# Performance work log

Hardware: AMD Instinct MI355X
Metric: run time of the kernel (lower is better)

The kernel has to match this reference:

```python
import jax, jax.numpy as jnp
import numpy as np

EMB_DIM = 1024
HEAD_SIZE = 128
B, T = 8, 2048


def setup_inputs() -> dict:
    key = jax.random.key(0)
    kx, kk, kq, kv = jax.random.split(key, 4)
    x = jax.random.normal(kx, (B, T, EMB_DIM), dtype=jnp.float32)
    # torch nn.Linear(emb_dim, head_size, bias=False): weight [head_size, emb_dim], y = x @ W.T
    # store transposed as [emb_dim, head_size] for direct matmul
    s = 1.0 / np.sqrt(EMB_DIM)
    Wk = jax.random.uniform(kk, (EMB_DIM, HEAD_SIZE), dtype=jnp.float32, minval=-s, maxval=s)
    Wq = jax.random.uniform(kq, (EMB_DIM, HEAD_SIZE), dtype=jnp.float32, minval=-s, maxval=s)
    Wv = jax.random.uniform(kv, (EMB_DIM, HEAD_SIZE), dtype=jnp.float32, minval=-s, maxval=s)
    return {"x": x, "Wk": Wk, "Wq": Wq, "Wv": Wv}


def reference(x, Wk, Wq, Wv):
    Bb, Tt, C = x.shape
    k = jnp.einsum('btc,ch->bth', x, Wk)
    q = jnp.einsum('btc,ch->bth', x, Wq)
    v = jnp.einsum('btc,ch->bth', x, Wv)
    # NOTE: original computes k @ q^T (not q @ k^T) and scales by C**-0.5 (C = emb_dim)
    wei = jnp.einsum('bih,bjh->bij', k, q) * (C ** -0.5)  # [B, T, T]
    causal = jnp.tril(jnp.ones((Tt, Tt), dtype=bool))
    wei = jnp.where(causal, wei, -jnp.inf)
    wei = jax.nn.softmax(wei, axis=-1)
    out = jnp.einsum('bij,bjh->bih', wei, v)  # [B, T, head_size]
    return out
```

## Files before the change

kernel.cpp:

```cpp
#include <hip/hip_runtime.h>
#include <hip/hip_bf16.h>
#include <stdint.h>

#define Bn 8
#define Tn 2048
#define Cn 1024
#define Hn 128

typedef __attribute__((ext_vector_type(8))) short short8;
typedef __attribute__((ext_vector_type(4))) short short4v;
typedef __attribute__((ext_vector_type(4))) float f32x4;
typedef __attribute__((ext_vector_type(4))) int int4v;

static __device__ __forceinline__ unsigned short f2bf(float f) {
    union { float f; unsigned int u; } v; v.f = f;
    return (unsigned short)((v.u + 0x7FFFu + ((v.u >> 16) & 1u)) >> 16);
}
static __device__ __forceinline__ float bf2f(unsigned short h) {
    union { unsigned int u; float f; } v; v.u = ((unsigned int)h) << 16;
    return v.f;
}

#define KSCALE 0.04508422f

#define BASE_BYTES (3u * Bn * Tn * Hn * 2u + 3u * Hn * Cn * 2u)
#define SLOT_SH 2080
#define NBLK_FA 576
#define UPB_FA 72
#define CCHUNK 8

__global__ __launch_bounds__(256) void wt_prep(const float* __restrict__ Wk,
                                               const float* __restrict__ Wq,
                                               const float* __restrict__ Wv,
                                               unsigned short* __restrict__ WT) {
    int z = blockIdx.y;
    const float* W = (z == 0) ? Wk : (z == 1) ? Wq : Wv;
    unsigned short* wt = WT + (size_t)z * Hn * Cn;
    int o = blockIdx.x * 256 + threadIdx.x;
    int d = o >> 10;
    int k = o & (Cn - 1);
    wt[o] = f2bf(W[k * Hn + d]);
}

__global__ __launch_bounds__(256) void proj4(const float* __restrict__ x,
                                             const unsigned short* __restrict__ WTb,
                                             unsigned short* __restrict__ Kb,
                                             unsigned short* __restrict__ Qb,
                                             unsigned short* __restrict__ VT) {
    __shared__ __align__(16) unsigned short Asm[2][32 * 32];
    __shared__ __align__(16) unsigned short Bsm[2][384 * 32];
    int tid = threadIdx.x;
    int lane = tid & 63, w = tid >> 6;
    int lr = lane & 15, lg = lane >> 4;
    int r0 = blockIdx.x * 32;

    f32x4 xreg;
    int4v breg[6];
    int xrow = tid >> 3, xk4 = (tid & 7) * 4;
    int brow = tid >> 2, bk8 = (tid & 3) * 8;
    auto LOADS = [&](int k0) {
        xreg = *(const f32x4*)(x + (size_t)(r0 + xrow) * Cn + k0 + xk4);
        #pragma unroll
        for (int i = 0; i < 6; ++i)
            breg[i] = *(const int4v*)(WTb + (size_t)(i * 64 + brow) * Cn + k0 + bk8);
    };
    auto WRITES = [&](int bb) {
        short4v av;
        av[0] = (short)f2bf(xreg[0]); av[1] = (short)f2bf(xreg[1]);
        av[2] = (short)f2bf(xreg[2]); av[3] = (short)f2bf(xreg[3]);
        *(short4v*)((char*)&Asm[bb][0] + xrow * 64 + xk4 * 2) = av;
        char* bbase = (char*)&Bsm[bb][0];
        #pragma unroll
        for (int i = 0; i < 6; ++i)
            *(int4v*)(bbase + (i * 64 + brow) * 64 + bk8 * 2) = breg[i];
    };

    f32x4 acc[2][6] = {};
    LOADS(0);
    WRITES(0);
    __syncthreads();
    int cur = 0;
    for (int ks = 0; ks < 32; ++ks) {
        if (ks < 31) LOADS((ks + 1) * 32);
        const char* ab = (const char*)&Asm[cur][0];
        const char* bbp = (const char*)&Bsm[cur][0];
        short8 af[2], bf[6];
        #pragma unroll
        for (int m = 0; m < 2; ++m)
            af[m] = *(const short8*)(ab + (m * 16 + lr) * 64 + lg * 16);
        #pragma unroll
        for (int c = 0; c < 6; ++c)
            bf[c] = *(const short8*)(bbp + (w * 96 + c * 16 + lr) * 64 + lg * 16);
        #pragma unroll
        for (int m = 0; m < 2; ++m)
            #pragma unroll
            for (int c = 0; c < 6; ++c)
                acc[m][c] = __builtin_amdgcn_mfma_f32_16x16x32_bf16(af[m], bf[c], acc[m][c], 0, 0, 0);
        if (ks < 31) WRITES(cur ^ 1);
        __syncthreads();
        cur ^= 1;
    }

    #pragma unroll
    for (int m = 0; m < 2; ++m)
        #pragma unroll
        for (int c = 0; c < 6; ++c) {
            int col = w * 96 + c * 16 + lr;
            int z = col >> 7, d = col & 127;
            if (z == 2) {
                int i = r0 + m * 16 + lg * 4;
                int bb = i >> 11, tt = i & 2047;
                short4v pv;
                pv[0] = (short)f2bf(acc[m][c][0]);
                pv[1] = (short)f2bf(acc[m][c][1]);
                pv[2] = (short)f2bf(acc[m][c][2]);
                pv[3] = (short)f2bf(acc[m][c][3]);
                *(short4v*)(VT + ((size_t)(bb * Hn + d) << 11) + tt) = pv;
            } else {
                unsigned short* outp = (z == 0) ? Kb : Qb;
                float sc = (z == 0) ? KSCALE : 1.0f;
                #pragma unroll
                for (int r = 0; r < 4; ++r) {
                    int i = r0 + m * 16 + lg * 4 + r;
                    outp[(size_t)i * Hn + d] = f2bf(acc[m][c][r] * sc);
                }
            }
        }
}

__global__ __launch_bounds__(512) void fattn8(const unsigned short* __restrict__ Kb,
                                              const unsigned short* __restrict__ Qb,
                                              const unsigned short* __restrict__ VT,
                                              unsigned short* __restrict__ accP) {
    __shared__ __align__(16) unsigned short Ksm[2][32 * 128];
    __shared__ __align__(16) unsigned short Vsm[2][128 * 32];
    __shared__ __align__(16) unsigned short pbuf[8][16][48];
    int tid = threadIdx.x, lane = tid & 63, w = tid >> 6;
    int lr = lane & 15, lg = lane >> 4;

    int cpx = gridDim.x >> 3;
    int u = ((int)blockIdx.x & 7) * cpx + ((int)blockIdx.x >> 3);
    int b = u / UPB_FA, rem = u - b * UPB_FA;
    int g = 0, p = 0;
    for (;;) {
        int P = (4 * g + 4 + CCHUNK - 1) / CCHUNK;
        if (rem < P) { p = rem; break; }
        rem -= P; ++g;
    }
    int nt = 4 * g + 4;
    int P = (nt + CCHUNK - 1) / CCHUNK;
    int q = nt / P, r = nt % P;
    int begin = p * q + (p < r ? p : r);
    int size = q + (p < r ? 1 : 0);

    int i0 = g * 128 + w * 16;
    int tmax = (i0 + 15) >> 5;
    const unsigned short* kb = Kb + (size_t)b * Tn * Hn;
    const unsigned short* qb = Qb + (size_t)b * Tn * Hn;
    const unsigned short* vt = VT + (size_t)b * Hn * Tn;

    short8 kf[4];
    #pragma unroll
    for (int kk = 0; kk < 4; ++kk)
        kf[kk] = *(const short8*)(kb + (size_t)(i0 + lr) * Hn + kk * 32 + lg * 8);

    int krow = tid >> 4, kcol = (tid & 15) * 8;
    int vrow = tid >> 2, vcol = (tid & 3) * 8;
    int4v kreg, vreg;
    auto LOADT = [&](int tt) {
        int j0 = tt * 32;
        kreg = *(const int4v*)(qb + (size_t)(j0 + krow) * Hn + kcol);
        vreg = *(const int4v*)(vt + (size_t)vrow * Tn + j0 + vcol);
    };
    auto WRITET = [&](int bb) {
        *(int4v*)((char*)&Ksm[bb][0] + krow * 256 + ((kcol * 2) ^ ((krow & 7) << 4))) = kreg;
        *(int4v*)((char*)&Vsm[bb][0] + vrow * 64 + vcol * 2) = vreg;
    };

    f32x4 acc[8] = {};
    float ssum[4] = {0.f, 0.f, 0.f, 0.f};

    LOADT(begin);
    WRITET(0);
    __syncthreads();
    int cur = 0;
    for (int ti = 0; ti < size; ++ti) {
        int tt = begin + ti;
        if (ti + 1 < size) LOADT(tt + 1);
        if (tt <= tmax) {
            int j0 = tt * 32;
            const char* kbp = (const char*)&Ksm[cur][0];
            const char* vbp = (const char*)&Vsm[cur][0];
            f32x4 sa0 = {}, sa1 = {};
            #pragma unroll
            for (int kk = 0; kk < 4; ++kk) {
                int row = lr;
                short8 qf = *(const short8*)(kbp + row * 256 + (((kk * 64) + lg * 16) ^ ((row & 7) << 4)));
                sa0 = __builtin_amdgcn_mfma_f32_16x16x32_bf16(kf[kk], qf, sa0, 0, 0, 0);
            }
            #pragma unroll
            for (int kk = 0; kk < 4; ++kk) {
                int row = 16 + lr;
                short8 qf = *(const short8*)(kbp + row * 256 + (((kk * 64) + lg * 16) ^ ((row & 7) << 4)));
                sa1 = __builtin_amdgcn_mfma_f32_16x16x32_bf16(kf[kk], qf, sa1, 0, 0, 0);
            }
            bool needmask = (j0 + 31 > i0);
            #pragma unroll
            for (int rr = 0; rr < 4; ++rr) {
                float v0 = sa0[rr], v1 = sa1[rr];
                if (needmask) {
                    int i = i0 + lg * 4 + rr;
                    if (j0 + lr > i)      v0 = -1e30f;
                    if (j0 + 16 + lr > i) v1 = -1e30f;
                }
                float p0 = __builtin_amdgcn_exp2f(v0);
                float p1 = __builtin_amdgcn_exp2f(v1);
                ssum[rr] += p0 + p1;
                pbuf[w][lg * 4 + rr][lr] = f2bf(p0);
                pbuf[w][lg * 4 + rr][16 + lr] = f2bf(p1);
            }
            short8 pf = *(const short8*)(&pbuf[w][lr][lg * 8]);
            #pragma unroll
            for (int n = 0; n < 8; ++n) {
                int row = n * 16 + lr;
                short8 vf = *(const short8*)(vbp + row * 64 + lg * 16);
                acc[n] = __builtin_amdgcn_mfma_f32_16x16x32_bf16(pf, vf, acc[n], 0, 0, 0);
            }
        }
        if (ti + 1 < size) WRITET(cur ^ 1);
        __syncthreads();
        cur ^= 1;
    }

    unsigned short* dst = accP + (size_t)u * 8 * SLOT_SH + (size_t)w * SLOT_SH;
    #pragma unroll
    for (int n = 0; n < 8; ++n) {
        short4v pv;
        pv[0] = (short)f2bf(acc[n][0]);
        pv[1] = (short)f2bf(acc[n][1]);
        pv[2] = (short)f2bf(acc[n][2]);
        pv[3] = (short)f2bf(acc[n][3]);
        *(short4v*)(dst + n * 256 + lane * 4) = pv;
    }
    #pragma unroll
    for (int rr = 0; rr < 4; ++rr) {
        float s = ssum[rr];
        s += __shfl_xor(s, 1);
        s += __shfl_xor(s, 2);
        s += __shfl_xor(s, 4);
        s += __shfl_xor(s, 8);
        if (lr == 0) ((float*)(dst + 2048))[lg * 4 + rr] = s;
    }
}

__global__ __launch_bounds__(256) void combine3(const unsigned short* __restrict__ accP,
                                                float* __restrict__ out) {
    int cpx = gridDim.x >> 3;
    int bidx = ((int)blockIdx.x & 7) * cpx + ((int)blockIdx.x >> 3);
    int b = bidx >> 7, tile = bidx & 127;
    int g = tile >> 3, wq = tile & 7;
    int ub = b * UPB_FA;
    for (int gg = 0; gg < g; ++gg) ub += (4 * gg + 4 + CCHUNK - 1) / CCHUNK;
    int nt = 4 * g + 4;
    int P = (nt + CCHUNK - 1) / CCHUNK;

    int tid = threadIdx.x;
    int row = tid >> 4;
    int c8 = (tid & 15) * 8;

    const unsigned short* base = accP + ((size_t)ub * 8 + wq) * SLOT_SH;
    const size_t pstr = (size_t)8 * SLOT_SH;
    float den = 0.f;
    for (int pp = 0; pp < P; ++pp) den += ((const float*)(base + pp * pstr + 2048))[row];
    float inv = 1.0f / den;

    int lgg = row >> 2, r4 = row & 3;
    float ov[8];
    #pragma unroll
    for (int cc = 0; cc < 8; ++cc) {
        int col = c8 + cc;
        int n = col >> 4, lrr = col & 15;
        int flat = n * 256 + (lgg * 16 + lrr) * 4 + r4;
        float s = 0.f;
        for (int pp = 0; pp < P; ++pp) s += bf2f(base[pp * pstr + flat]);
        ov[cc] = s * inv;
    }
    float* op = out + ((size_t)(b * Tn + tile * 16 + row)) * Hn + c8;
    *(f32x4*)op       = f32x4{ov[0], ov[1], ov[2], ov[3]};
    *(f32x4*)(op + 4) = f32x4{ov[4], ov[5], ov[6], ov[7]};
}

__global__ __launch_bounds__(256) void attn(const unsigned short* __restrict__ Kb,
                                            const unsigned short* __restrict__ Qb,
                                            const unsigned short* __restrict__ VT,
                                            float* __restrict__ out) {
    __shared__ unsigned short pbuf[4][16][32];
    __shared__ __align__(16) float accbuf[4][16][132];
    __shared__ float ssbuf[4][16];
    int lane = threadIdx.x & 63;
    int w = threadIdx.x >> 6;
    int b = blockIdx.y;
    int xb = blockIdx.x;
    int tile = (xb & 1) ? (127 - (xb >> 1)) : (xb >> 1);
    int i0 = tile * 16;
    int lr = lane & 15, lg = lane >> 4;

    const unsigned short* kb = Kb + (size_t)b * Tn * Hn;
    const unsigned short* qb = Qb + (size_t)b * Tn * Hn;
    const unsigned short* vt = VT + (size_t)b * Hn * Tn;

    short8 kf[4];
    #pragma unroll
    for (int kk = 0; kk < 4; ++kk)
        kf[kk] = *(const short8*)(kb + (size_t)(i0 + lr) * Hn + kk * 32 + lg * 8);

    f32x4 acc[8] = {};
    float ssum[4] = {0.f, 0.f, 0.f, 0.f};

    int nt = (i0 + 15) / 32 + 1;
    for (int tt = w; tt < nt; tt += 4) {
        int j0 = tt * 32;
        f32x4 sa0 = {}, sa1 = {};
        #pragma unroll
        for (int kk = 0; kk < 4; ++kk) {
            short8 q0 = *(const short8*)(qb + (size_t)(j0 + lr) * Hn + kk * 32 + lg * 8);
            sa0 = __builtin_amdgcn_mfma_f32_16x16x32_bf16(kf[kk], q0, sa0, 0, 0, 0);
        }
        #pragma unroll
        for (int kk = 0; kk < 4; ++kk) {
            short8 q1 = *(const short8*)(qb + (size_t)(j0 + 16 + lr) * Hn + kk * 32 + lg * 8);
            sa1 = __builtin_amdgcn_mfma_f32_16x16x32_bf16(kf[kk], q1, sa1, 0, 0, 0);
        }
        bool needmask = (j0 + 31 > i0);
        #pragma unroll
        for (int r = 0; r < 4; ++r) {
            float v0 = sa0[r], v1 = sa1[r];
            if (needmask) {
                int i = i0 + lg * 4 + r;
                if (j0 + lr > i)      v0 = -1e30f;
                if (j0 + 16 + lr > i) v1 = -1e30f;
            }
            float p0 = __builtin_amdgcn_exp2f(v0);
            float p1 = __builtin_amdgcn_exp2f(v1);
            ssum[r] += p0 + p1;
            pbuf[w][lg * 4 + r][lr] = f2bf(p0);
            pbuf[w][lg * 4 + r][16 + lr] = f2bf(p1);
        }
        short8 pf = *(const short8*)(&pbuf[w][lr][lg * 8]);
        #pragma unroll
        for (int n = 0; n < 8; ++n) {
            short8 vf = *(const short8*)(vt + (size_t)(n * 16 + lr) * Tn + j0 + lg * 8);
            acc[n] = __builtin_amdgcn_mfma_f32_16x16x32_bf16(pf, vf, acc[n], 0, 0, 0);
        }
    }

    #pragma unroll
    for (int r = 0; r < 4; ++r) {
        float s = ssum[r];
        s += __shfl_xor(s, 1);
        s += __shfl_xor(s, 2);
        s += __shfl_xor(s, 4);
        s += __shfl_xor(s, 8);
        if (lr == 0) ssbuf[w][lg * 4 + r] = s;
    }
    #pragma unroll
    for (int n = 0; n < 8; ++n)
        #pragma unroll
        for (int r = 0; r < 4; ++r)
            accbuf[w][lg * 4 + r][n * 16 + lr] = acc[n][r];
    __syncthreads();

    int row = threadIdx.x >> 5;
    int col = (threadIdx.x & 31) * 4;
    #pragma unroll
    for (int h = 0; h < 2; ++h) {
        int rr = row + h * 8;
        f32x4 s = *(const f32x4*)(&accbuf[0][rr][col]);
        #pragma unroll
        for (int ww = 1; ww < 4; ++ww) {
            f32x4 t = *(const f32x4*)(&accbuf[ww][rr][col]);
            s[0] += t[0]; s[1] += t[1]; s[2] += t[2]; s[3] += t[3];
        }
        float den = ssbuf[0][rr] + ssbuf[1][rr] + ssbuf[2][rr] + ssbuf[3][rr];
        float inv = 1.0f / den;
        s[0] *= inv; s[1] *= inv; s[2] *= inv; s[3] *= inv;
        *(f32x4*)(&out[((size_t)(b * Tn + i0 + rr)) * Hn + col]) = s;
    }
}

extern "C" void kernel_launch(void* const* d_in, const int* in_sizes, int n_in,
                              void* d_out, int out_size, void* d_ws, size_t ws_size,
                              hipStream_t stream) {
    const float* x  = (const float*)d_in[0];
    const float* Wk = (const float*)d_in[1];
    const float* Wq = (const float*)d_in[2];
    const float* Wv = (const float*)d_in[3];

    unsigned short* Kb = (unsigned short*)d_ws;
    unsigned short* Qb = Kb + (size_t)Bn * Tn * Hn;
    unsigned short* VT = Qb + (size_t)Bn * Tn * Hn;
    unsigned short* WT = VT + (size_t)Bn * Tn * Hn;
    unsigned short* accP = (unsigned short*)((char*)d_ws + BASE_BYTES);

    wt_prep<<<dim3(512, 3), 256, 0, stream>>>(Wk, Wq, Wv, WT);
    proj4<<<dim3(512), 256, 0, stream>>>(x, WT, Kb, Qb, VT);

    const size_t need = (size_t)BASE_BYTES + (size_t)NBLK_FA * 8 * SLOT_SH * 2;
    if (ws_size >= need) {
        fattn8<<<dim3(NBLK_FA), 512, 0, stream>>>(Kb, Qb, VT, accP);
        combine3<<<dim3(1024), 256, 0, stream>>>(accP, (float*)d_out);
    } else {
        attn<<<dim3(128, 8), 256, 0, stream>>>(Kb, Qb, VT, (float*)d_out);
    }
}
```

Measured before the change: 86.78 us.

## Retile QKV projection with async global-to-LDS loads and in-register bf16 conversion

Measured after the change: 83.47 us. 3.8% less time.

```diff
diff --git a/kernel.cpp b/kernel.cpp
--- a/kernel.cpp
+++ b/kernel.cpp
@@ -19,6 +19,22 @@
 static __device__ __forceinline__ float bf2f(unsigned short h) {
     union { unsigned int u; float f; } v; v.u = ((unsigned int)h) << 16;
     return v.f;
+}
+
+static __device__ __forceinline__ short8 cvt8(f32x4 a, f32x4 b) {
+    union { unsigned int u[4]; short8 s; } r;
+    asm("v_cvt_pk_bf16_f32 %0, %1, %2" : "=v"(r.u[0]) : "v"(a[0]), "v"(a[1]));
+    asm("v_cvt_pk_bf16_f32 %0, %1, %2" : "=v"(r.u[1]) : "v"(a[2]), "v"(a[3]));
+    asm("v_cvt_pk_bf16_f32 %0, %1, %2" : "=v"(r.u[2]) : "v"(b[0]), "v"(b[1]));
+    asm("v_cvt_pk_bf16_f32 %0, %1, %2" : "=v"(r.u[3]) : "v"(b[2]), "v"(b[3]));
+    return r.s;
+}
+
+static __device__ __forceinline__ void async16(const void* g, void* l) {
+    __builtin_amdgcn_global_load_lds(
+        (const __attribute__((address_space(1))) unsigned int*)g,
+        (__attribute__((address_space(3))) unsigned int*)l,
+        16, 0, 0);
 }
 
 #define KSCALE 0.04508422f
@@ -42,90 +58,100 @@
     wt[o] = f2bf(W[k * Hn + d]);
 }
 
-__global__ __launch_bounds__(256) void proj4(const float* __restrict__ x,
+__global__ __launch_bounds__(256) void proj6(const float* __restrict__ x,
                                              const unsigned short* __restrict__ WTb,
                                              unsigned short* __restrict__ Kb,
                                              unsigned short* __restrict__ Qb,
                                              unsigned short* __restrict__ VT) {
-    __shared__ __align__(16) unsigned short Asm[2][32 * 32];
-    __shared__ __align__(16) unsigned short Bsm[2][384 * 32];
+    __shared__ __align__(16) unsigned short Bsm[2][128 * 32];
+    __shared__ __align__(16) float Asm[2][64 * 32];
     int tid = threadIdx.x;
     int lane = tid & 63, w = tid >> 6;
     int lr = lane & 15, lg = lane >> 4;
-    int r0 = blockIdx.x * 32;
-
-    f32x4 xreg;
-    int4v breg[6];
-    int xrow = tid >> 3, xk4 = (tid & 7) * 4;
-    int brow = tid >> 2, bk8 = (tid & 3) * 8;
-    auto LOADS = [&](int k0) {
-        xreg = *(const f32x4*)(x + (size_t)(r0 + xrow) * Cn + k0 + xk4);
-        #pragma unroll
-        for (int i = 0; i < 6; ++i)
-            breg[i] = *(const int4v*)(WTb + (size_t)(i * 64 + brow) * Cn + k0 + bk8);
+    int wm = w >> 1, wn = w & 1;
+
+    int u = ((int)(blockIdx.x & 7)) * 96 + ((int)blockIdx.x >> 3);
+    int rg = u / 3, cg = u - rg * 3;
+    int r0 = rg * 64;
+    const unsigned short* WTz = WTb + (size_t)cg * Hn * Cn;
+
+    int br_in = lane >> 2;
+    int bc8 = (lane & 3) * 8;
+    int ar_in = lane >> 3;
+    int aspos = lane & 7;
+
+    auto STAGE = [&](int bb, int k0) {
+        #pragma unroll
+        for (int i = 0; i < 2; ++i) {
+            int ch = w * 2 + i;
+            int brow = ch * 16 + br_in;
+            async16(WTz + (size_t)brow * Cn + k0 + bc8, &Bsm[bb][ch * 512]);
+            int arow = ch * 8 + ar_in;
+            int ac = aspos ^ (arow & 7);
+            async16(x + (size_t)(r0 + arow) * Cn + k0 + ac * 4, &Asm[bb][ch * 256]);
+        }
     };
-    auto WRITES = [&](int bb) {
-        short4v av;
-        av[0] = (short)f2bf(xreg[0]); av[1] = (short)f2bf(xreg[1]);
-        av[2] = (short)f2bf(xreg[2]); av[3] = (short)f2bf(xreg[3]);
-        *(short4v*)((char*)&Asm[bb][0] + xrow * 64 + xk4 * 2) = av;
-        char* bbase = (char*)&Bsm[bb][0];
-        #pragma unroll
-        for (int i = 0; i < 6; ++i)
-            *(int4v*)(bbase + (i * 64 + brow) * 64 + bk8 * 2) = breg[i];
-    };
-
-    f32x4 acc[2][6] = {};
-    LOADS(0);
-    WRITES(0);
+
+    f32x4 acc[2][4] = {};
+    STAGE(0, 0);
     __syncthreads();
     int cur = 0;
     for (int ks = 0; ks < 32; ++ks) {
-        if (ks < 31) LOADS((ks + 1) * 32);
-        const char* ab = (const char*)&Asm[cur][0];
-        const char* bbp = (const char*)&Bsm[cur][0];
-        short8 af[2], bf[6];
+        if (ks < 31) STAGE(cur ^ 1, (ks + 1) * 32);
+        short8 af[2], bf[4];
+        #pragma unroll
+        for (int m = 0; m < 2; ++m) {
+            int arow = wm * 32 + m * 16 + lr;
+            const char* abase = (const char*)&Asm[cur][arow * 32];
+            f32x4 a0 = *(const f32x4*)(abase + ((((lg * 2)    ) ^ (arow & 7)) << 4));
+            f32x4 a1 = *(const f32x4*)(abase + ((((lg * 2) + 1) ^ (arow & 7)) << 4));
+            af[m] = cvt8(a0, a1);
+        }
+        #pragma unroll
+        for (int c = 0; c < 4; ++c) {
+            int brow = wn * 64 + c * 16 + lr;
+            bf[c] = *(const short8*)(&Bsm[cur][brow * 32 + lg * 8]);
+        }
         #pragma unroll
         for (int m = 0; m < 2; ++m)
-            af[m] = *(const short8*)(ab + (m * 16 + lr) * 64 + lg * 16);
-        #pragma unroll
-        for (int c = 0; c < 6; ++c)
-            bf[c] = *(const short8*)(bbp + (w * 96 + c * 16 + lr) * 64 + lg * 16);
-        #pragma unroll
-        for (int m = 0; m < 2; ++m)
-            #pragma unroll
-            for (int c = 0; c < 6; ++c)
+            #pragma unroll
+            for (int c = 0; c < 4; ++c)
                 acc[m][c] = __builtin_amdgcn_mfma_f32_16x16x32_bf16(af[m], bf[c], acc[m][c], 0, 0, 0);
-        if (ks < 31) WRITES(cur ^ 1);
         __syncthreads();
         cur ^= 1;
     }
 
-    #pragma unroll
-    for (int m = 0; m < 2; ++m)
-        #pragma unroll
-        for (int c = 0; c < 6; ++c) {
-            int col = w * 96 + c * 16 + lr;
-            int z = col >> 7, d = col & 127;
-            if (z == 2) {
-                int i = r0 + m * 16 + lg * 4;
-                int bb = i >> 11, tt = i & 2047;
+    if (cg == 2) {
+        int bb = r0 >> 11;
+        int tb = r0 & 2047;
+        #pragma unroll
+        for (int m = 0; m < 2; ++m)
+            #pragma unroll
+            for (int c = 0; c < 4; ++c) {
+                int d = wn * 64 + c * 16 + lr;
+                int t = tb + wm * 32 + m * 16 + lg * 4;
                 short4v pv;
                 pv[0] = (short)f2bf(acc[m][c][0]);
                 pv[1] = (short)f2bf(acc[m][c][1]);
                 pv[2] = (short)f2bf(acc[m][c][2]);
                 pv[3] = (short)f2bf(acc[m][c][3]);
-                *(short4v*)(VT + ((size_t)(bb * Hn + d) << 11) + tt) = pv;
-            } else {
-                unsigned short* outp = (z == 0) ? Kb : Qb;
-                float sc = (z == 0) ? KSCALE : 1.0f;
+                *(short4v*)(VT + ((size_t)(bb * Hn + d) << 11) + t) = pv;
+            }
+    } else {
+        unsigned short* outp = (cg == 0) ? Kb : Qb;
+        float sc = (cg == 0) ? KSCALE : 1.0f;
+        #pragma unroll
+        for (int m = 0; m < 2; ++m)
+            #pragma unroll
+            for (int c = 0; c < 4; ++c) {
+                int d = wn * 64 + c * 16 + lr;
                 #pragma unroll
                 for (int r = 0; r < 4; ++r) {
-                    int i = r0 + m * 16 + lg * 4 + r;
+                    int i = r0 + wm * 32 + m * 16 + lg * 4 + r;
                     outp[(size_t)i * Hn + d] = f2bf(acc[m][c][r] * sc);
                 }
             }
-        }
+    }
 }
 
 __global__ __launch_bounds__(512) void fattn8(const unsigned short* __restrict__ Kb,
@@ -403,7 +429,7 @@
     unsigned short* accP = (unsigned short*)((char*)d_ws + BASE_BYTES);
 
     wt_prep<<<dim3(512, 3), 256, 0, stream>>>(Wk, Wq, Wv, WT);
-    proj4<<<dim3(512), 256, 0, stream>>>(x, WT, Kb, Qb, VT);
+    proj6<<<dim3(768), 256, 0, stream>>>(x, WT, Kb, Qb, VT);
 
     const size_t need = (size_t)BASE_BYTES + (size_t)NBLK_FA * 8 * SLOT_SH * 2;
     if (ws_size >= need) {
```
